# Performance work log

Measured on AMD Instinct MI355X. Metric: run time of the kernel, lower is better.

## Reference

```python
import jax, jax.numpy as jnp
import numpy as np

N = 4096          # n_assets
D_MODEL = 512
DK = 128
EMB_DIM = 32
QC = 4.0          # quantization_coeff
NUM_EMB = int(np.floor((N - 1) / QC)) + 1  # 1024


def setup_inputs() -> dict:
    key = jax.random.key(0)
    ks = jax.random.split(key, 9)

    def lin_w(k, out_d, in_d):
        # torch nn.Linear default init ~ U(-1/sqrt(in_d), 1/sqrt(in_d))
        b = 1.0 / np.sqrt(in_d)
        return jax.random.uniform(k, (out_d, in_d), jnp.float32, -b, b)

    return {
        "stock_reprs": jax.random.normal(ks[0], (N, D_MODEL), jnp.float32),
        "price_rising_ranks": jax.random.uniform(ks[1], (N,), jnp.float32, 0.0, float(N)),
        "Wq_w": lin_w(ks[2], DK, D_MODEL), "Wq_b": jnp.zeros((DK,), jnp.float32),
        "Wk_w": lin_w(ks[3], DK, D_MODEL), "Wk_b": jnp.zeros((DK,), jnp.float32),
        "Wv_w": lin_w(ks[4], D_MODEL, D_MODEL), "Wv_b": jnp.zeros((D_MODEL,), jnp.float32),
        "rank_emb": jax.random.normal(ks[5], (NUM_EMB, EMB_DIM), jnp.float32),
        "wL_w": lin_w(ks[6], 1, EMB_DIM), "wL_b": jnp.zeros((1,), jnp.float32),
        "wf_w": lin_w(ks[7], 1, D_MODEL), "wf_b": jnp.zeros((1,), jnp.float32),
    }


def reference(stock_reprs, price_rising_ranks, Wq_w, Wq_b, Wk_w, Wk_b,
              Wv_w, Wv_b, rank_emb, wL_w, wL_b, wf_w, wf_b):
    # QKV projections: [N, dk], [N, dk], [N, d_model]
    q = stock_reprs @ Wq_w.T + Wq_b
    k = stock_reprs @ Wk_w.T + Wk_b
    v = stock_reprs @ Wv_w.T + Wv_b

    # Quantized pairwise rank-distance indices [N, N]
    diff = jnp.abs(price_rising_ranks[:, None] - price_rising_ranks[None, :])
    d_ij = jnp.clip(jnp.floor(diff / QC).astype(jnp.int32), 0, NUM_EMB - 1)

    # Gate per quantized distance: sigmoid(w_L(Emb[d])). Precompute the
    # [NUM_EMB] table instead of materializing the [N, N, EMB_DIM] gather
    # (same math: the lookup-then-linear commutes with the gather).
    gate_table = jax.nn.sigmoid(rank_emb @ wL_w[0] + wL_b[0])  # [NUM_EMB]
    psi = gate_table[d_ij]                                     # [N, N]

    score = (q @ k.T) / np.sqrt(float(DK))                     # [N, N]
    att = jax.nn.softmax(psi * score, axis=-1)                 # [N, N]
    a = att @ v                                                # [N, d_model]
    return jax.nn.sigmoid(a @ wf_w[0] + wf_b[0])               # [N]
```

## Files before the change

kernel.cpp:

```cpp
#include <hip/hip_runtime.h>
#include <hip/hip_bf16.h>

#define N_ASSETS 4096
#define DMODEL 512
#define DKQ 128
#define NUM_EMB 1024

#define SCLQ 0.12752789f

typedef float f32x4 __attribute__((ext_vector_type(4)));
typedef short s16x8 __attribute__((ext_vector_type(8)));

__device__ __forceinline__ unsigned short f2bf(float x) {
    unsigned u = __float_as_uint(x);
    u += 0x7FFF + ((u >> 16) & 1);
    return (unsigned short)(u >> 16);
}

__device__ __forceinline__ unsigned pk2(float lo, float hi) {
    __hip_bfloat162 h = __float22bfloat162_rn(make_float2(lo, hi));
    return *(unsigned*)&h;
}

__device__ __forceinline__ s16x8 ld8(const unsigned short* p) {
    return *(const s16x8*)p;
}

__global__ __launch_bounds__(256) void k_prep(const float* __restrict__ remb,
                                              const float* __restrict__ wLw,
                                              const float* __restrict__ wLb,
                                              const float* __restrict__ Wq,
                                              const float* __restrict__ Wk,
                                              const float* __restrict__ bq,
                                              const float* __restrict__ bk,
                                              const float* __restrict__ Wv,
                                              const float* __restrict__ bv,
                                              const float* __restrict__ wfw,
                                              float* __restrict__ gate,
                                              unsigned short* __restrict__ Wb,
                                              float* __restrict__ bias,
                                              float* __restrict__ weff) {
    int bid = blockIdx.x;
    int tid = threadIdx.x;
    if (bid < 4) {
        int e = bid * 256 + tid;
        float s = wLb[0];
#pragma unroll
        for (int j = 0; j < 32; ++j) s += remb[e * 32 + j] * wLw[j];
        gate[e] = 1.f / (1.f + __expf(-s));
    } else if (bid < 132) {
        int gid = (bid - 4) * 256 + tid;
        int i4 = gid * 4;
        int row = i4 >> 9;
        int col = i4 & 511;
        const float* src; int r;
        if (row < 128) { src = Wq; r = row; } else { src = Wk; r = row - 128; }
        float4 v = *(const float4*)(src + r * 512 + col);
        ushort4 o;
        o.x = f2bf(v.x); o.y = f2bf(v.y); o.z = f2bf(v.z); o.w = f2bf(v.w);
        *(ushort4*)(Wb + i4) = o;
        if (gid < 256) bias[gid] = (gid < 128) ? bq[gid] : bk[gid - 128];
    } else if (bid < 148) {
        __shared__ float wf_s[512];
        __shared__ float part[8][32];
        wf_s[tid] = wfw[tid];
        wf_s[tid + 256] = wfw[tid + 256];
        __syncthreads();
        int din = (bid - 132) * 32 + (tid & 31);
        int slice = tid >> 5;
        const float* wp = Wv + din;
        float a = 0.f;
#pragma unroll 4
        for (int j = 0; j < 64; ++j) {
            int dout = slice * 64 + j;
            a += wp[(size_t)dout * 512] * wf_s[dout];
        }
        part[slice][tid & 31] = a;
        __syncthreads();
        if (tid < 32) {
            float s = 0.f;
#pragma unroll
            for (int sl = 0; sl < 8; ++sl) s += part[sl][tid];
            weff[(bid - 132) * 32 + tid] = s;
        }
    } else {
        if (tid < 64) {
            float s = 0.f;
#pragma unroll
            for (int j = 0; j < 8; ++j) s += bv[tid * 8 + j] * wfw[tid * 8 + j];
#pragma unroll
            for (int m = 1; m < 64; m <<= 1) s += __shfl_xor(s, m);
            if (tid == 0) weff[512] = s;
        }
    }
}

__global__ __launch_bounds__(256) void k_proj(const float* __restrict__ X,
                                              const float* __restrict__ weff,
                                              const unsigned short* __restrict__ Wb,
                                              const float* __restrict__ bias,
                                              unsigned short* __restrict__ qb,
                                              unsigned short* __restrict__ kb,
                                              float* __restrict__ u) {
    int tid = threadIdx.x;
    int lane = tid & 63, w = tid >> 6;
    int l15 = lane & 15, lhi = lane >> 4;
    int m0 = blockIdx.x * 16;

    const float* xrow = X + (size_t)(m0 + l15) * DMODEL + lhi * 8;
    const float* wrow = weff + lhi * 8;

    s16x8 af[16];
    float us = 0.f;
    bool dou = (w == 0);
#pragma unroll
    for (int kc = 0; kc < 16; ++kc) {
        float4 a = *(const float4*)(xrow + kc * 32);
        float4 b = *(const float4*)(xrow + kc * 32 + 4);
        if (dou) {
            float4 wa = *(const float4*)(wrow + kc * 32);
            float4 wb = *(const float4*)(wrow + kc * 32 + 4);
            us += a.x * wa.x + a.y * wa.y + a.z * wa.z + a.w * wa.w
                + b.x * wb.x + b.y * wb.y + b.z * wb.z + b.w * wb.w;
        }
        union { s16x8 v; unsigned q[4]; } fr;
        fr.q[0] = pk2(a.x, a.y);
        fr.q[1] = pk2(a.z, a.w);
        fr.q[2] = pk2(b.x, b.y);
        fr.q[3] = pk2(b.z, b.w);
        af[kc] = fr.v;
    }
    if (dou) {
        us += __shfl_xor(us, 16);
        us += __shfl_xor(us, 32);
        if (lane < 16) u[m0 + lane] = us + weff[512];
    }

    int n0w = w * 64;
    f32x4 zero4 = {0.f, 0.f, 0.f, 0.f};
    f32x4 acc[4];
#pragma unroll
    for (int ni = 0; ni < 4; ++ni) acc[ni] = zero4;

#pragma unroll
    for (int k0 = 0; k0 < 16; ++k0) {
#pragma unroll
        for (int ni = 0; ni < 4; ++ni) {
            s16x8 bf = ld8(Wb + (size_t)(n0w + ni * 16 + l15) * 512 + k0 * 32 + lhi * 8);
            acc[ni] = __builtin_amdgcn_mfma_f32_16x16x32_bf16(af[k0], bf, acc[ni], 0, 0, 0);
        }
    }

#pragma unroll
    for (int ni = 0; ni < 4; ++ni) {
        int n = n0w + ni * 16 + l15;
        float bv_ = bias[n];
#pragma unroll
        for (int r = 0; r < 4; ++r) {
            int m = m0 + lhi * 4 + r;
            float v = acc[ni][r] + bv_;
            if (n < 128) qb[m * 128 + n] = f2bf(v * SCLQ);
            else         kb[m * 128 + (n - 128)] = f2bf(v);
        }
    }
}

__global__ __launch_bounds__(256) void k_score(const unsigned short* __restrict__ qb,
                                               const unsigned short* __restrict__ kb,
                                               const float* __restrict__ ranks,
                                               const float* __restrict__ gate,
                                               const float* __restrict__ u,
                                               float* __restrict__ num_part,
                                               float* __restrict__ den_part) {
    __shared__ float g_lds[NUM_EMB];
    __shared__ float rr[128], rc[128], uc[128];
    int tid = threadIdx.x;
    int lane = tid & 63, w = tid >> 6;
    int l15 = lane & 15, lhi = lane >> 4;
    int wm = w >> 1, wn = w & 1;
    int bm = blockIdx.x, bn = blockIdx.y;

    for (int i = tid; i < NUM_EMB; i += 256) g_lds[i] = gate[i];
    if (tid < 128) {
        rr[tid] = ranks[bm * 128 + tid];
        rc[tid] = ranks[bn * 128 + tid];
        uc[tid] = u[bn * 128 + tid];
    }
    __syncthreads();

    int row0 = wm * 64;
    int col0 = wn * 64;

    f32x4 zero4 = {0.f, 0.f, 0.f, 0.f};
    f32x4 acc[4][4];
#pragma unroll
    for (int mi = 0; mi < 4; ++mi)
#pragma unroll
        for (int ni = 0; ni < 4; ++ni) acc[mi][ni] = zero4;

#pragma unroll
    for (int k0 = 0; k0 < DKQ; k0 += 32) {
        s16x8 af[4], bf[4];
#pragma unroll
        for (int mi = 0; mi < 4; ++mi)
            af[mi] = ld8(qb + (bm * 128 + row0 + mi * 16 + l15) * DKQ + k0 + lhi * 8);
#pragma unroll
        for (int ni = 0; ni < 4; ++ni)
            bf[ni] = ld8(kb + (bn * 128 + col0 + ni * 16 + l15) * DKQ + k0 + lhi * 8);
#pragma unroll
        for (int mi = 0; mi < 4; ++mi)
#pragma unroll
            for (int ni = 0; ni < 4; ++ni)
                acc[mi][ni] = __builtin_amdgcn_mfma_f32_16x16x32_bf16(af[mi], bf[ni], acc[mi][ni], 0, 0, 0);
    }

    float num[4][4], den[4][4];
#pragma unroll
    for (int mi = 0; mi < 4; ++mi)
#pragma unroll
        for (int r = 0; r < 4; ++r) { num[mi][r] = 0.f; den[mi][r] = 0.f; }

#pragma unroll
    for (int mi = 0; mi < 4; ++mi) {
#pragma unroll
        for (int ni = 0; ni < 4; ++ni) {
            int coll = col0 + ni * 16 + l15;
            float rj = rc[coll];
            float uj = uc[coll];
#pragma unroll
            for (int r = 0; r < 4; ++r) {
                int rowl = row0 + mi * 16 + lhi * 4 + r;
                float diff = fabsf(rr[rowl] - rj);
                int d = min((int)(diff * 0.25f), NUM_EMB - 1);
                float p = exp2f(g_lds[d] * acc[mi][ni][r]);
                den[mi][r] += p;
                num[mi][r] += p * uj;
            }
        }
    }
#pragma unroll
    for (int mi = 0; mi < 4; ++mi) {
#pragma unroll
        for (int r = 0; r < 4; ++r) {
            float vn = num[mi][r], vd = den[mi][r];
            vn += __shfl_xor(vn, 1); vd += __shfl_xor(vd, 1);
            vn += __shfl_xor(vn, 2); vd += __shfl_xor(vd, 2);
            vn += __shfl_xor(vn, 4); vd += __shfl_xor(vd, 4);
            vn += __shfl_xor(vn, 8); vd += __shfl_xor(vd, 8);
            if (l15 == 0) {
                int row = bm * 128 + row0 + mi * 16 + lhi * 4 + r;
                num_part[(bn * 2 + wn) * N_ASSETS + row] = vn;
                den_part[(bn * 2 + wn) * N_ASSETS + row] = vd;
            }
        }
    }
}

__global__ __launch_bounds__(256) void k_out(const float* __restrict__ num_part,
                                             const float* __restrict__ den_part,
                                             const float* __restrict__ wfb,
                                             float* __restrict__ out) {
    int lane = threadIdx.x & 63, w = threadIdx.x >> 6;
    int row = blockIdx.x * 4 + w;
    float vn = num_part[lane * N_ASSETS + row];
    float vd = den_part[lane * N_ASSETS + row];
#pragma unroll
    for (int m = 1; m < 64; m <<= 1) {
        vn += __shfl_xor(vn, m);
        vd += __shfl_xor(vd, m);
    }
    if (lane == 0) out[row] = 1.f / (1.f + __expf(-(vn / vd + wfb[0])));
}

extern "C" void kernel_launch(void* const* d_in, const int* in_sizes, int n_in,
                              void* d_out, int out_size, void* d_ws, size_t ws_size,
                              hipStream_t stream) {
    const float* X    = (const float*)d_in[0];
    const float* rks  = (const float*)d_in[1];
    const float* Wq_w = (const float*)d_in[2];
    const float* Wq_b = (const float*)d_in[3];
    const float* Wk_w = (const float*)d_in[4];
    const float* Wk_b = (const float*)d_in[5];
    const float* Wv_w = (const float*)d_in[6];
    const float* Wv_b = (const float*)d_in[7];
    const float* remb = (const float*)d_in[8];
    const float* wL_w = (const float*)d_in[9];
    const float* wL_b = (const float*)d_in[10];
    const float* wf_w = (const float*)d_in[11];
    const float* wf_b = (const float*)d_in[12];
    float* out = (float*)d_out;
    char* ws = (char*)d_ws;

    const size_t OFF_GATE = 0;
    const size_t OFF_BIAS = 4096;
    const size_t OFF_WEFF = 8192;
    const size_t OFF_WB   = 12288;
    const size_t OFF_QB   = OFF_WB + 262144;
    const size_t OFF_KB   = OFF_QB + 1048576;
    const size_t OFF_U    = OFF_KB + 1048576;
    const size_t OFF_NUM  = OFF_U + 16384;
    const size_t OFF_DEN  = OFF_NUM + 1048576;

    float* gate = (float*)(ws + OFF_GATE);
    float* bias = (float*)(ws + OFF_BIAS);
    float* weff = (float*)(ws + OFF_WEFF);
    unsigned short* Wb = (unsigned short*)(ws + OFF_WB);
    unsigned short* qb = (unsigned short*)(ws + OFF_QB);
    unsigned short* kb = (unsigned short*)(ws + OFF_KB);
    float* u = (float*)(ws + OFF_U);
    float* num_part = (float*)(ws + OFF_NUM);
    float* den_part = (float*)(ws + OFF_DEN);

    k_prep<<<149, 256, 0, stream>>>(remb, wL_w, wL_b, Wq_w, Wk_w, Wq_b, Wk_b,
                                    Wv_w, Wv_b, wf_w, gate, Wb, bias, weff);
    k_proj<<<256, 256, 0, stream>>>(X, weff, Wb, bias, qb, kb, u);
    k_score<<<dim3(32, 32), 256, 0, stream>>>(qb, kb, rks, gate, u, num_part, den_part);
    k_out<<<1024, 256, 0, stream>>>(num_part, den_part, wf_b, out);
}
```

Measured before the change: 71.73 us.

## Coalesce weff reduction, split projection N across blocks, transpose partial sums

The Wv·wf reduction now uses four blocks that each read contiguous float2 rows and write four partial vectors, which k_proj sums on the fly. k_proj gets a second grid dimension so each block computes half the output columns, doubling block count. k_score caches row ranks in registers, and the num/den partials are stored row-major so k_out reads them contiguously. The costs are that X is loaded and converted twice in k_proj, and the k_score partial writes become strided.

```diff
diff --git a/kernel.cpp b/kernel.cpp
--- a/kernel.cpp
+++ b/kernel.cpp
@@ -39,7 +39,7 @@
                                               float* __restrict__ gate,
                                               unsigned short* __restrict__ Wb,
                                               float* __restrict__ bias,
-                                              float* __restrict__ weff) {
+                                              float* __restrict__ weff4) {
     int bid = blockIdx.x;
     int tid = threadIdx.x;
     if (bid < 4) {
@@ -60,29 +60,19 @@
         o.x = f2bf(v.x); o.y = f2bf(v.y); o.z = f2bf(v.z); o.w = f2bf(v.w);
         *(ushort4*)(Wb + i4) = o;
         if (gid < 256) bias[gid] = (gid < 128) ? bq[gid] : bk[gid - 128];
-    } else if (bid < 148) {
-        __shared__ float wf_s[512];
-        __shared__ float part[8][32];
-        wf_s[tid] = wfw[tid];
-        wf_s[tid + 256] = wfw[tid + 256];
-        __syncthreads();
-        int din = (bid - 132) * 32 + (tid & 31);
-        int slice = tid >> 5;
-        const float* wp = Wv + din;
-        float a = 0.f;
-#pragma unroll 4
-        for (int j = 0; j < 64; ++j) {
-            int dout = slice * 64 + j;
-            a += wp[(size_t)dout * 512] * wf_s[dout];
-        }
-        part[slice][tid & 31] = a;
-        __syncthreads();
-        if (tid < 32) {
-            float s = 0.f;
-#pragma unroll
-            for (int sl = 0; sl < 8; ++sl) s += part[sl][tid];
-            weff[(bid - 132) * 32 + tid] = s;
-        }
+    } else if (bid < 136) {
+        int dbase = (bid - 132) * 128;
+        float a0 = 0.f, a1 = 0.f;
+        const float* wp = Wv + (size_t)dbase * 512 + tid * 2;
+#pragma unroll 8
+        for (int j = 0; j < 128; ++j) {
+            float wfv = wfw[dbase + j];
+            float2 v = *(const float2*)(wp + (size_t)j * 512);
+            a0 += v.x * wfv;
+            a1 += v.y * wfv;
+        }
+        weff4[(bid - 132) * 512 + tid * 2] = a0;
+        weff4[(bid - 132) * 512 + tid * 2 + 1] = a1;
     } else {
         if (tid < 64) {
             float s = 0.f;
@@ -90,13 +80,13 @@
             for (int j = 0; j < 8; ++j) s += bv[tid * 8 + j] * wfw[tid * 8 + j];
 #pragma unroll
             for (int m = 1; m < 64; m <<= 1) s += __shfl_xor(s, m);
-            if (tid == 0) weff[512] = s;
+            if (tid == 0) weff4[2048] = s;
         }
     }
 }
 
 __global__ __launch_bounds__(256) void k_proj(const float* __restrict__ X,
-                                              const float* __restrict__ weff,
+                                              const float* __restrict__ weff4,
                                               const unsigned short* __restrict__ Wb,
                                               const float* __restrict__ bias,
                                               unsigned short* __restrict__ qb,
@@ -106,22 +96,37 @@
     int lane = tid & 63, w = tid >> 6;
     int l15 = lane & 15, lhi = lane >> 4;
     int m0 = blockIdx.x * 16;
+    int n0w = blockIdx.y * 128 + w * 32;
 
     const float* xrow = X + (size_t)(m0 + l15) * DMODEL + lhi * 8;
-    const float* wrow = weff + lhi * 8;
 
     s16x8 af[16];
     float us = 0.f;
-    bool dou = (w == 0);
+    bool dou = (w == 0) && (blockIdx.y == 0);
 #pragma unroll
     for (int kc = 0; kc < 16; ++kc) {
         float4 a = *(const float4*)(xrow + kc * 32);
         float4 b = *(const float4*)(xrow + kc * 32 + 4);
         if (dou) {
-            float4 wa = *(const float4*)(wrow + kc * 32);
-            float4 wb = *(const float4*)(wrow + kc * 32 + 4);
-            us += a.x * wa.x + a.y * wa.y + a.z * wa.z + a.w * wa.w
-                + b.x * wb.x + b.y * wb.y + b.z * wb.z + b.w * wb.w;
+            int off = kc * 32 + lhi * 8;
+            float4 p0 = *(const float4*)(weff4 + off);
+            float4 p1 = *(const float4*)(weff4 + 512 + off);
+            float4 p2 = *(const float4*)(weff4 + 1024 + off);
+            float4 p3 = *(const float4*)(weff4 + 1536 + off);
+            float4 q0 = *(const float4*)(weff4 + off + 4);
+            float4 q1 = *(const float4*)(weff4 + 512 + off + 4);
+            float4 q2 = *(const float4*)(weff4 + 1024 + off + 4);
+            float4 q3 = *(const float4*)(weff4 + 1536 + off + 4);
+            float wax = p0.x + p1.x + p2.x + p3.x;
+            float way = p0.y + p1.y + p2.y + p3.y;
+            float waz = p0.z + p1.z + p2.z + p3.z;
+            float waw = p0.w + p1.w + p2.w + p3.w;
+            float wbx = q0.x + q1.x + q2.x + q3.x;
+            float wby = q0.y + q1.y + q2.y + q3.y;
+            float wbz = q0.z + q1.z + q2.z + q3.z;
+            float wbw = q0.w + q1.w + q2.w + q3.w;
+            us += a.x * wax + a.y * way + a.z * waz + a.w * waw
+                + b.x * wbx + b.y * wby + b.z * wbz + b.w * wbw;
         }
         union { s16x8 v; unsigned q[4]; } fr;
         fr.q[0] = pk2(a.x, a.y);
@@ -133,26 +138,25 @@
     if (dou) {
         us += __shfl_xor(us, 16);
         us += __shfl_xor(us, 32);
-        if (lane < 16) u[m0 + lane] = us + weff[512];
-    }
-
-    int n0w = w * 64;
+        if (lane < 16) u[m0 + lane] = us + weff4[2048];
+    }
+
     f32x4 zero4 = {0.f, 0.f, 0.f, 0.f};
-    f32x4 acc[4];
-#pragma unroll
-    for (int ni = 0; ni < 4; ++ni) acc[ni] = zero4;
+    f32x4 acc[2];
+#pragma unroll
+    for (int ni = 0; ni < 2; ++ni) acc[ni] = zero4;
 
 #pragma unroll
     for (int k0 = 0; k0 < 16; ++k0) {
 #pragma unroll
-        for (int ni = 0; ni < 4; ++ni) {
+        for (int ni = 0; ni < 2; ++ni) {
             s16x8 bf = ld8(Wb + (size_t)(n0w + ni * 16 + l15) * 512 + k0 * 32 + lhi * 8);
             acc[ni] = __builtin_amdgcn_mfma_f32_16x16x32_bf16(af[k0], bf, acc[ni], 0, 0, 0);
         }
     }
 
 #pragma unroll
-    for (int ni = 0; ni < 4; ++ni) {
+    for (int ni = 0; ni < 2; ++ni) {
         int n = n0w + ni * 16 + l15;
         float bv_ = bias[n];
 #pragma unroll
@@ -214,6 +218,12 @@
                 acc[mi][ni] = __builtin_amdgcn_mfma_f32_16x16x32_bf16(af[mi], bf[ni], acc[mi][ni], 0, 0, 0);
     }
 
+    float rreg[4][4];
+#pragma unroll
+    for (int mi = 0; mi < 4; ++mi)
+#pragma unroll
+        for (int r = 0; r < 4; ++r) rreg[mi][r] = rr[row0 + mi * 16 + lhi * 4 + r];
+
     float num[4][4], den[4][4];
 #pragma unroll
     for (int mi = 0; mi < 4; ++mi)
@@ -229,8 +239,7 @@
             float uj = uc[coll];
 #pragma unroll
             for (int r = 0; r < 4; ++r) {
-                int rowl = row0 + mi * 16 + lhi * 4 + r;
-                float diff = fabsf(rr[rowl] - rj);
+                float diff = fabsf(rreg[mi][r] - rj);
                 int d = min((int)(diff * 0.25f), NUM_EMB - 1);
                 float p = exp2f(g_lds[d] * acc[mi][ni][r]);
                 den[mi][r] += p;
@@ -238,6 +247,7 @@
             }
         }
     }
+    int slot = bn * 2 + wn;
 #pragma unroll
     for (int mi = 0; mi < 4; ++mi) {
 #pragma unroll
@@ -249,8 +259,8 @@
             vn += __shfl_xor(vn, 8); vd += __shfl_xor(vd, 8);
             if (l15 == 0) {
                 int row = bm * 128 + row0 + mi * 16 + lhi * 4 + r;
-                num_part[(bn * 2 + wn) * N_ASSETS + row] = vn;
-                den_part[(bn * 2 + wn) * N_ASSETS + row] = vd;
+                num_part[row * 64 + slot] = vn;
+                den_part[row * 64 + slot] = vd;
             }
         }
     }
@@ -262,8 +272,8 @@
                                              float* __restrict__ out) {
     int lane = threadIdx.x & 63, w = threadIdx.x >> 6;
     int row = blockIdx.x * 4 + w;
-    float vn = num_part[lane * N_ASSETS + row];
-    float vd = den_part[lane * N_ASSETS + row];
+    float vn = num_part[row * 64 + lane];
+    float vd = den_part[row * 64 + lane];
 #pragma unroll
     for (int m = 1; m < 64; m <<= 1) {
         vn += __shfl_xor(vn, m);
@@ -291,19 +301,19 @@
     float* out = (float*)d_out;
     char* ws = (char*)d_ws;
 
-    const size_t OFF_GATE = 0;
-    const size_t OFF_BIAS = 4096;
-    const size_t OFF_WEFF = 8192;
-    const size_t OFF_WB   = 12288;
-    const size_t OFF_QB   = OFF_WB + 262144;
-    const size_t OFF_KB   = OFF_QB + 1048576;
-    const size_t OFF_U    = OFF_KB + 1048576;
-    const size_t OFF_NUM  = OFF_U + 16384;
-    const size_t OFF_DEN  = OFF_NUM + 1048576;
+    const size_t OFF_GATE  = 0;
+    const size_t OFF_BIAS  = 4096;
+    const size_t OFF_WEFF4 = 8192;
+    const size_t OFF_WB    = 20480;
+    const size_t OFF_QB    = OFF_WB + 262144;
+    const size_t OFF_KB    = OFF_QB + 1048576;
+    const size_t OFF_U     = OFF_KB + 1048576;
+    const size_t OFF_NUM   = OFF_U + 16384;
+    const size_t OFF_DEN   = OFF_NUM + 1048576;
 
     float* gate = (float*)(ws + OFF_GATE);
     float* bias = (float*)(ws + OFF_BIAS);
-    float* weff = (float*)(ws + OFF_WEFF);
+    float* weff4 = (float*)(ws + OFF_WEFF4);
     unsigned short* Wb = (unsigned short*)(ws + OFF_WB);
     unsigned short* qb = (unsigned short*)(ws + OFF_QB);
     unsigned short* kb = (unsigned short*)(ws + OFF_KB);
@@ -311,9 +321,9 @@
     float* num_part = (float*)(ws + OFF_NUM);
     float* den_part = (float*)(ws + OFF_DEN);
 
-    k_prep<<<149, 256, 0, stream>>>(remb, wL_w, wL_b, Wq_w, Wk_w, Wq_b, Wk_b,
-                                    Wv_w, Wv_b, wf_w, gate, Wb, bias, weff);
-    k_proj<<<256, 256, 0, stream>>>(X, weff, Wb, bias, qb, kb, u);
+    k_prep<<<137, 256, 0, stream>>>(remb, wL_w, wL_b, Wq_w, Wk_w, Wq_b, Wk_b,
+                                    Wv_w, Wv_b, wf_w, gate, Wb, bias, weff4);
+    k_proj<<<dim3(256, 2), 256, 0, stream>>>(X, weff4, Wb, bias, qb, kb, u);
     k_score<<<dim3(32, 32), 256, 0, stream>>>(qb, kb, rks, gate, u, num_part, den_part);
     k_out<<<1024, 256, 0, stream>>>(num_part, den_part, wf_b, out);
 }
```

Result: faster. 60.18 us (-16.1%).
